# Kernel optimization log

Hardware: AMD Instinct MI355X
Metric: run time of the kernel (lower is better)

## Reference

```python
import jax, jax.numpy as jnp
import numpy as np

BS, EMB, RES = 256, 768, 14
N_MASKS, HID, OUT, N_PROJ = 16, 4096, 256, 4
BN_EPS = 1e-5


def setup_inputs() -> dict:
    key = jax.random.key(0)
    ks = jax.random.split(key, 8)
    x = jax.random.normal(ks[0], (BS, EMB, RES, RES), jnp.float32)
    # binary ROI masks over the 14x14 = 196 patch grid
    masks = (jax.random.uniform(ks[1], (BS, N_MASKS, RES * RES)) < 0.3).astype(jnp.float32)
    projection_idx = jax.random.randint(ks[2], (N_MASKS,), 0, N_PROJ, jnp.int32)
    mask_ids = jax.random.randint(ks[3], (BS, N_MASKS), 0, 100, jnp.int32)
    # stacked params for the N_PROJ MLP projectors
    W1 = jax.random.normal(ks[4], (N_PROJ, EMB, HID), jnp.float32) * 0.02
    b1 = jnp.zeros((N_PROJ, HID), jnp.float32)
    gamma = jnp.ones((N_PROJ, HID), jnp.float32)
    beta = jnp.zeros((N_PROJ, HID), jnp.float32)
    W2 = jax.random.normal(ks[5], (N_PROJ, HID, OUT), jnp.float32) * 0.02
    b2 = jnp.zeros((N_PROJ, OUT), jnp.float32)
    return {"x": x, "masks": masks, "projection_idx": projection_idx,
            "mask_ids": mask_ids, "W1": W1, "b1": b1, "gamma": gamma,
            "beta": beta, "W2": W2, "b2": b2}


def reference(x, masks, projection_idx, mask_ids, W1, b1, gamma, beta, W2, b2):
    bs, emb, hx, hy = x.shape
    # [bs, emb, hx, hy] -> [bs, hw, emb]
    emb_local = jnp.transpose(x, (0, 2, 3, 1)).reshape(bs, hx * hy, emb)
    # mask-normalized pooling:  pooled[b,n,:] = mean of embeddings inside mask n
    area = masks.sum(axis=-1, keepdims=True)
    smpl = masks / jnp.maximum(area, 1.0)
    pooled = smpl @ emb_local                       # [bs, n_masks, emb]
    # dense dispatch: run EVERY projector over all pooled tokens (as original)
    h = jnp.einsum('bne,peh->pbnh', pooled, W1) + b1[:, None, None, :]
    # BatchNorm1d in training mode over flattened (bs*n_masks) batch, per projector
    mu = h.mean(axis=(1, 2), keepdims=True)
    var = jnp.mean(jnp.square(h - mu), axis=(1, 2), keepdims=True)  # biased var
    h = (h - mu) * jax.lax.rsqrt(var + BN_EPS) * gamma[:, None, None, :] + beta[:, None, None, :]
    h = jax.nn.relu(h)
    o = jnp.einsum('pbnh,pho->pbno', h, W2) + b2[:, None, None, :]   # [P, bs, n, out]
    # keep only projector projection_idx[n] for mask-slot n (disjoint selection)
    n_proj = W1.shape[0]
    sel = (projection_idx[None, :] == jnp.arange(n_proj)[:, None]).astype(o.dtype)  # [P, n]
    xs = (o * sel[:, None, :, None]).sum(axis=0)     # [bs, n_masks, out]
    return (xs, mask_ids)
```

## Files before the change

### kernel.cpp

```cpp
#include <hip/hip_runtime.h>
#include <hip/hip_bf16.h>

#define BS 256
#define EMB 768
#define HW 196
#define NMASK 16
#define HID 4096
#define OUT 256
#define NPROJ 4
#define MROWS 4096

typedef __attribute__((ext_vector_type(8))) short bf16x8;
typedef __attribute__((ext_vector_type(4))) float f32x4;
typedef __attribute__((ext_vector_type(8))) unsigned short u16x8;

__device__ inline float bf2f(unsigned short u) {
    unsigned int x = ((unsigned int)u) << 16;
    return __builtin_bit_cast(float, x);
}
__device__ inline short f2bfs(float f) {
    return __builtin_bit_cast(short, __float2bfloat16(f));
}

#define GL16(gptr, lptr)                                                     \
    __builtin_amdgcn_global_load_lds(                                        \
        (const __attribute__((address_space(1))) void*)(gptr),               \
        (__attribute__((address_space(3))) void*)(lptr), 16, 0, 0)

__global__ __launch_bounds__(256) void fused_k1(
    const float* __restrict__ x, const float* __restrict__ masks,
    const float* __restrict__ W1, const float* __restrict__ W2,
    __hip_bfloat16* __restrict__ pooledG,
    __hip_bfloat16* __restrict__ W1T, __hip_bfloat16* __restrict__ W2T,
    float* __restrict__ mpB)
{
    __shared__ __align__(16) char smu[16704];
    const int bid = blockIdx.x, tid = threadIdx.x;

    if (bid < 1024) {
        short* afr = (short*)smu;
        float* inv = (float*)(smu + 14592);
        const int ec = bid & 3, b = bid >> 2;
        const float* mb = masks + (size_t)b * NMASK * HW;

        for (int s = tid; s < 7 * 64; s += 256) {
            int m = s & 15, kb = ((s >> 4) & 3) * 8 + (s >> 6) * 32;
            short v[8];
            #pragma unroll
            for (int j = 0; j < 8; ++j) {
                int kk = kb + j;
                v[j] = (kk < HW) ? f2bfs(mb[m * HW + kk]) : (short)0;
            }
            #pragma unroll
            for (int j = 0; j < 8; ++j) afr[s * 8 + j] = v[j];
        }
        if (tid >= 192) {
            int l = tid - 192, m = l >> 2, q = l & 3;
            float a = 0.f;
            for (int hw = q; hw < HW; hw += 4) a += mb[m * HW + hw];
            a += __shfl_xor(a, 1);
            a += __shfl_xor(a, 2);
            if (q == 0) inv[m] = 1.0f / fmaxf(a, 1.0f);
        }
        __syncthreads();

        const int lane = tid & 63, w = tid >> 6;
        const int lc = lane & 15, l4 = lane >> 4;
        const int ebase = ec * 192 + w * 48;
        const bf16x8* afv = (const bf16x8*)afr;
        f32x4 acc[3] = {};

        const float* xb0 = x + ((size_t)b * EMB + ebase + lc) * HW;

        for (int kc = 0; kc < 6; ++kc) {
            bf16x8 af = afv[kc * 64 + lane];
            float4 u[3][2];
            #pragma unroll
            for (int t = 0; t < 3; ++t) {
                const float* xr = xb0 + (size_t)(t * 16) * HW + kc * 32 + l4 * 8;
                u[t][0] = *(const float4*)(xr);
                u[t][1] = *(const float4*)(xr + 4);
            }
            #pragma unroll
            for (int t = 0; t < 3; ++t) {
                bf16x8 bf;
                bf[0] = f2bfs(u[t][0].x); bf[1] = f2bfs(u[t][0].y);
                bf[2] = f2bfs(u[t][0].z); bf[3] = f2bfs(u[t][0].w);
                bf[4] = f2bfs(u[t][1].x); bf[5] = f2bfs(u[t][1].y);
                bf[6] = f2bfs(u[t][1].z); bf[7] = f2bfs(u[t][1].w);
                acc[t] = __builtin_amdgcn_mfma_f32_16x16x32_bf16(af, bf, acc[t], 0, 0, 0);
            }
        }
        {
            bf16x8 af = afv[6 * 64 + lane];
            #pragma unroll
            for (int t = 0; t < 3; ++t) {
                bf16x8 bf = {};
                if (l4 == 0) {
                    float4 u0 = *(const float4*)(xb0 + (size_t)(t * 16) * HW + 192);
                    bf[0] = f2bfs(u0.x); bf[1] = f2bfs(u0.y);
                    bf[2] = f2bfs(u0.z); bf[3] = f2bfs(u0.w);
                }
                acc[t] = __builtin_amdgcn_mfma_f32_16x16x32_bf16(af, bf, acc[t], 0, 0, 0);
            }
        }

        #pragma unroll
        for (int t = 0; t < 3; ++t) {
            int e = ebase + t * 16 + lc;
            float msum = 0.f;
            #pragma unroll
            for (int j = 0; j < 4; ++j) {
                int m = l4 * 4 + j;
                float v = acc[t][j] * inv[m];
                msum += v;
                pooledG[((size_t)m * 256 + b) * EMB + e] = __float2bfloat16(v);
            }
            msum += __shfl_xor(msum, 16);
            msum += __shfl_xor(msum, 32);
            if (l4 == 0) mpB[(size_t)b * EMB + e] = msum;
        }
    } else {
        const float* src; __hip_bfloat16* dst; int R, C, xx, yy, z;
        if (bid < 4096) { int idx = bid - 1024; z = idx / 768; int r = idx % 768;
                          xx = r % 64; yy = r / 64; src = W1; dst = W1T; R = EMB; C = HID; }
        else            { int idx = bid - 4096; z = idx / 256; int r = idx % 256;
                          xx = r % 4;  yy = r / 4;  src = W2; dst = W2T; R = HID; C = OUT; }
        float (*tile)[65] = (float(*)[65])smu;
        const float* s = src + (size_t)z * R * C;
        __hip_bfloat16* d = dst + (size_t)z * R * C;
        const int c0 = xx * 64, r0 = yy * 64;
        for (int i = tid; i < 4096; i += 256) {
            int r = i >> 6, c = i & 63;
            tile[r][c] = s[(size_t)(r0 + r) * C + c0 + c];
        }
        __syncthreads();
        for (int i = tid; i < 4096; i += 256) {
            int c = i >> 6, r = i & 63;
            d[(size_t)(c0 + c) * R + r0 + r] = __float2bfloat16(tile[r][c]);
        }
    }
}

__global__ __launch_bounds__(256) void pgT_kernel(
    const __hip_bfloat16* __restrict__ src, __hip_bfloat16* __restrict__ dst)
{
    __shared__ __hip_bfloat16 tile[64][65];
    const int c0 = blockIdx.x * 64, r0 = blockIdx.y * 64, tid = threadIdx.x;
    for (int i = tid; i < 4096; i += 256) {
        int r = i >> 6, c = i & 63;
        tile[r][c] = src[(size_t)(r0 + r) * EMB + c0 + c];
    }
    __syncthreads();
    for (int i = tid; i < 4096; i += 256) {
        int c = i >> 6, r = i & 63;
        dst[(size_t)(c0 + c) * MROWS + r0 + r] = tile[r][c];
    }
}

__global__ __launch_bounds__(256) void cgemm(
    const __hip_bfloat16* __restrict__ PT, float* __restrict__ Cpart)
{
    __shared__ __align__(16) __hip_bfloat16 As[128 * 32];
    __shared__ __align__(16) __hip_bfloat16 Bs[128 * 32];
    const int tid = threadIdx.x, lane = tid & 63, wid = tid >> 6;
    const int n0 = blockIdx.x * 128, m0 = blockIdx.y * 128, kbase = blockIdx.z * 512;
    float* Cp = Cpart + (size_t)blockIdx.z * EMB * EMB;
    const int wr = wid >> 1, wc = wid & 1;
    const int l4 = lane >> 4, lc = lane & 15;

    f32x4 acc[4][4] = {};
    for (int k0 = kbase; k0 < kbase + 512; k0 += 32) {
        __syncthreads();
        #pragma unroll
        for (int r = 0; r < 2; ++r) {
            int t = r * 256 + tid;
            int row = t >> 2, ko = (t & 3) * 8;
            GL16(PT + (size_t)(m0 + row) * MROWS + k0 + ko, &As[(r * 256 + wid * 64) * 8]);
        }
        #pragma unroll
        for (int r = 0; r < 2; ++r) {
            int t = r * 256 + tid;
            int row = t >> 2, ko = (t & 3) * 8;
            GL16(PT + (size_t)(n0 + row) * MROWS + k0 + ko, &Bs[(r * 256 + wid * 64) * 8]);
        }
        __syncthreads();
        const bf16x8* Av = (const bf16x8*)As;
        const bf16x8* Bv = (const bf16x8*)Bs;
        bf16x8 a[4], b[4];
        #pragma unroll
        for (int m = 0; m < 4; ++m) a[m] = Av[(wr * 64 + m * 16 + lc) * 4 + l4];
        #pragma unroll
        for (int n = 0; n < 4; ++n) b[n] = Bv[(wc * 64 + n * 16 + lc) * 4 + l4];
        #pragma unroll
        for (int m = 0; m < 4; ++m)
            #pragma unroll
            for (int n = 0; n < 4; ++n)
                acc[m][n] = __builtin_amdgcn_mfma_f32_16x16x32_bf16(a[m], b[n], acc[m][n], 0, 0, 0);
    }
    #pragma unroll
    for (int m = 0; m < 4; ++m)
        #pragma unroll
        for (int n = 0; n < 4; ++n)
            #pragma unroll
            for (int j = 0; j < 4; ++j) {
                int row = m0 + wr * 64 + m * 16 + l4 * 4 + j;
                int col = n0 + wc * 64 + n * 16 + lc;
                Cp[(size_t)row * EMB + col] = acc[m][n][j];
            }
}

__global__ __launch_bounds__(256) void cvt_c(
    const float* __restrict__ Cpart, const float* __restrict__ mpB,
    __hip_bfloat16* __restrict__ Cbf, float* __restrict__ mp)
{
    const int bid = blockIdx.x, tid = threadIdx.x;
    if (bid < 576) {
        int i = (bid * 256 + tid) * 4;
        float sx = 0.f, sy = 0.f, sz = 0.f, sw = 0.f;
        #pragma unroll
        for (int kz = 0; kz < 8; ++kz) {
            float4 v = *(const float4*)(Cpart + (size_t)kz * EMB * EMB + i);
            sx += v.x; sy += v.y; sz += v.z; sw += v.w;
        }
        const float s = 1.0f / 4096.0f;
        Cbf[i + 0] = __float2bfloat16(sx * s);
        Cbf[i + 1] = __float2bfloat16(sy * s);
        Cbf[i + 2] = __float2bfloat16(sz * s);
        Cbf[i + 3] = __float2bfloat16(sw * s);
    } else {
        int e = (bid - 576) * 256 + tid;
        float s = 0.f;
        for (int b = 0; b < 256; ++b) s += mpB[(size_t)b * EMB + e];
        mp[e] = s * (1.0f / 4096.0f);
    }
}

__global__ __launch_bounds__(256) void ugemm(
    const __hip_bfloat16* __restrict__ W1T, const __hip_bfloat16* __restrict__ Cbf,
    const float* __restrict__ mp,
    float* __restrict__ Eh2p, float* __restrict__ Mup)
{
    __shared__ __align__(16) __hip_bfloat16 As[128 * 32];
    __shared__ __align__(16) __hip_bfloat16 Bs[128 * 32];
    const int tid = threadIdx.x, lane = tid & 63, wid = tid >> 6;
    const int n0 = blockIdx.x * 128, m0 = blockIdx.y * 128, p = blockIdx.z;
    const __hip_bfloat16* Ap = W1T + (size_t)p * HID * EMB;
    const int wr = wid >> 1, wc = wid & 1;
    const int l4 = lane >> 4, lc = lane & 15;

    f32x4 acc[4][4] = {};
    for (int k0 = 0; k0 < EMB; k0 += 32) {
        __syncthreads();
        #pragma unroll
        for (int r = 0; r < 2; ++r) {
            int t = r * 256 + tid;
            int row = t >> 2, ko = (t & 3) * 8;
            GL16(Ap + (size_t)(m0 + row) * EMB + k0 + ko, &As[(r * 256 + wid * 64) * 8]);
        }
        #pragma unroll
        for (int r = 0; r < 2; ++r) {
            int t = r * 256 + tid;
            int row = t >> 2, ko = (t & 3) * 8;
            GL16(Cbf + (size_t)(n0 + row) * EMB + k0 + ko, &Bs[(r * 256 + wid * 64) * 8]);
        }
        __syncthreads();
        const bf16x8* Av = (const bf16x8*)As;
        const bf16x8* Bv = (const bf16x8*)Bs;
        bf16x8 a[4], b[4];
        #pragma unroll
        for (int m = 0; m < 4; ++m) a[m] = Av[(wr * 64 + m * 16 + lc) * 4 + l4];
        #pragma unroll
        for (int n = 0; n < 4; ++n) b[n] = Bv[(wc * 64 + n * 16 + lc) * 4 + l4];
        #pragma unroll
        for (int m = 0; m < 4; ++m)
            #pragma unroll
            for (int n = 0; n < 4; ++n)
                acc[m][n] = __builtin_amdgcn_mfma_f32_16x16x32_bf16(a[m], b[n], acc[m][n], 0, 0, 0);
    }

    float mpv[4];
    #pragma unroll
    for (int n = 0; n < 4; ++n) mpv[n] = mp[n0 + wc * 64 + n * 16 + lc];
    #pragma unroll
    for (int m = 0; m < 4; ++m) {
        #pragma unroll
        for (int j = 0; j < 4; ++j) {
            int row = m0 + wr * 64 + m * 16 + l4 * 4 + j;
            const __hip_bfloat16* wrow = Ap + (size_t)row * EMB;
            float e2 = 0.f, mu = 0.f;
            #pragma unroll
            for (int n = 0; n < 4; ++n) {
                int col = n0 + wc * 64 + n * 16 + lc;
                float wv = bf2f(__builtin_bit_cast(unsigned short, wrow[col]));
                e2 += acc[m][n][j] * wv;
                mu += mpv[n] * wv;
            }
            e2 += __shfl_xor(e2, 1); e2 += __shfl_xor(e2, 2);
            e2 += __shfl_xor(e2, 4); e2 += __shfl_xor(e2, 8);
            mu += __shfl_xor(mu, 1); mu += __shfl_xor(mu, 2);
            mu += __shfl_xor(mu, 4); mu += __shfl_xor(mu, 8);
            if (lc == 0) {
                size_t idx = (((size_t)blockIdx.x * 2 + wc) * NPROJ + p) * HID + row;
                Eh2p[idx] = e2;
                Mup [idx] = mu;
            }
        }
    }
}

__global__ __launch_bounds__(512, 2) void gemm1_sel(
    const __hip_bfloat16* __restrict__ A, const __hip_bfloat16* __restrict__ W1T,
    const int* __restrict__ proj,
    const float* __restrict__ Eh2p, const float* __restrict__ Mup,
    const float* __restrict__ gamma, const float* __restrict__ beta,
    __hip_bfloat16* __restrict__ hrelu)
{
    __shared__ __align__(16) short LS[3 * 16384];
    __shared__ float sS[256], sT[256];
    const int tid = threadIdx.x, lane = tid & 63, w = tid >> 6;
    const int wr = w >> 2, wc = w & 3;
    const int lc = lane & 15, l4 = lane >> 4;
    const int n0 = blockIdx.x * 256, m0 = blockIdx.y * 256;
    const int p = proj[blockIdx.y];
    const __hip_bfloat16* Ag = A;
    const __hip_bfloat16* Bg = W1T + (size_t)p * HID * EMB;
    const bf16x8* LSv = (const bf16x8*)LS;

    if (tid < 256) {
        int col = n0 + tid;
        float e2 = 0.f, mu = 0.f;
        #pragma unroll
        for (int s = 0; s < 12; ++s) {
            e2 += Eh2p[((size_t)s * NPROJ + p) * HID + col];
            mu += Mup [((size_t)s * NPROJ + p) * HID + col];
        }
        float var = e2 - mu * mu;
        float is  = rsqrtf(fmaxf(var, 0.0f) + 1e-5f);
        float sc  = gamma[p * HID + col] * is;
        sS[tid] = sc;
        sT[tid] = beta[p * HID + col] - mu * sc;
    }

    auto STAGE = [&](int t) {
        const int sb = (t % 3) * 32768;
        #pragma unroll
        for (int ab = 0; ab < 2; ++ab) {
            const __hip_bfloat16* g = ab ? Bg : Ag;
            const int rbase = ab ? n0 : m0;
            #pragma unroll
            for (int i = 0; i < 2; ++i) {
                int c = (w * 2 + i) * 64 + lane;
                int row = c >> 2, ps = c & 3;
                int ls = ps ^ (row & 3);
                const __hip_bfloat16* src =
                    g + (size_t)(rbase + row) * EMB + t * 32 + ls * 8;
                GL16(src, (char*)LS + sb + ab * 16384 + (w * 2 + i) * 1024);
            }
        }
    };

    f32x4 acc[8][4] = {};

    STAGE(0);
    STAGE(1);
    asm volatile("s_waitcnt vmcnt(4)" ::: "memory");
    __builtin_amdgcn_s_barrier();

    for (int t = 0; t < 24; ++t) {
        if (t + 2 < 24) STAGE(t + 2);
        const int vb = (t % 3) * 2048;

        bf16x8 bfr[4];
        #pragma unroll
        for (int nf = 0; nf < 4; ++nf) {
            int rb = wc * 64 + nf * 16 + lc;
            bfr[nf] = LSv[vb + 1024 + rb * 4 + (l4 ^ (rb & 3))];
        }
        #pragma unroll
        for (int q = 0; q < 4; ++q) {
            bf16x8 afr[2];
            #pragma unroll
            for (int m2 = 0; m2 < 2; ++m2) {
                int ra = wr * 128 + (q * 2 + m2) * 16 + lc;
                afr[m2] = LSv[vb + ra * 4 + (l4 ^ (ra & 3))];
            }
            __builtin_amdgcn_s_setprio(1);
            #pragma unroll
            for (int m2 = 0; m2 < 2; ++m2)
                #pragma unroll
                for (int nf = 0; nf < 4; ++nf)
                    acc[q * 2 + m2][nf] = __builtin_amdgcn_mfma_f32_16x16x32_bf16(
                        afr[m2], bfr[nf], acc[q * 2 + m2][nf], 0, 0, 0);
            __builtin_amdgcn_s_setprio(0);
        }

        if (t + 2 < 24) {
            asm volatile("s_waitcnt vmcnt(4)" ::: "memory");
            __builtin_amdgcn_s_barrier();
        } else if (t + 2 == 24) {
            asm volatile("s_waitcnt vmcnt(0)" ::: "memory");
            __builtin_amdgcn_s_barrier();
        }
    }

    #pragma unroll
    for (int nf = 0; nf < 4; ++nf) {
        int cl = wc * 64 + nf * 16 + lc;
        int col = n0 + cl;
        float s = sS[cl];
        float tt = sT[cl];
        #pragma unroll
        for (int mf = 0; mf < 8; ++mf)
            #pragma unroll
            for (int j = 0; j < 4; ++j) {
                int row = m0 + wr * 128 + mf * 16 + l4 * 4 + j;
                float v = fmaxf(acc[mf][nf][j] * s + tt, 0.0f);
                hrelu[(size_t)row * HID + col] = __float2bfloat16(v);
            }
    }
}

__global__ __launch_bounds__(256) void gemm2(
    const __hip_bfloat16* __restrict__ Hn, const __hip_bfloat16* __restrict__ W2T,
    const int* __restrict__ proj, float* __restrict__ Opart)
{
    __shared__ __align__(16) __hip_bfloat16 As[128 * 32];
    __shared__ __align__(16) __hip_bfloat16 Bs[128 * 32];
    const int tid = threadIdx.x, lane = tid & 63, wid = tid >> 6;
    const int nmask = blockIdx.x;
    const int bc    = blockIdx.y;
    const int ct    = blockIdx.z >> 2, kz = blockIdx.z & 3;
    const int p = proj[nmask];
    const __hip_bfloat16* Ap = Hn + (size_t)(nmask * 256 + bc * 128) * HID;
    const __hip_bfloat16* Bp = W2T + ((size_t)p * OUT + ct * 128) * HID;
    float* Op = Opart + (size_t)kz * MROWS * OUT;
    const int wr = wid >> 1, wc = wid & 1;
    const int l4 = lane >> 4, lc = lane & 15;

    f32x4 acc[4][4] = {};
    for (int k0 = kz * 1024; k0 < kz * 1024 + 1024; k0 += 32) {
        __syncthreads();
        #pragma unroll
        for (int r = 0; r < 2; ++r) {
            int t = r * 256 + tid;
            int row = t >> 2, ko = (t & 3) * 8;
            GL16(Ap + (size_t)row * HID + k0 + ko, &As[(r * 256 + wid * 64) * 8]);
        }
        #pragma unroll
        for (int r = 0; r < 2; ++r) {
            int t = r * 256 + tid;
            int row = t >> 2, ko = (t & 3) * 8;
            GL16(Bp + (size_t)row * HID + k0 + ko, &Bs[(r * 256 + wid * 64) * 8]);
        }
        __syncthreads();
        const bf16x8* Av = (const bf16x8*)As;
        const bf16x8* Bv = (const bf16x8*)Bs;
        bf16x8 a[4], b[4];
        #pragma unroll
        for (int m = 0; m < 4; ++m) a[m] = Av[(wr * 64 + m * 16 + lc) * 4 + l4];
        #pragma unroll
        for (int n = 0; n < 4; ++n) b[n] = Bv[(wc * 64 + n * 16 + lc) * 4 + l4];
        #pragma unroll
        for (int m = 0; m < 4; ++m)
            #pragma unroll
            for (int n = 0; n < 4; ++n)
                acc[m][n] = __builtin_amdgcn_mfma_f32_16x16x32_bf16(a[m], b[n], acc[m][n], 0, 0, 0);
    }

    #pragma unroll
    for (int m = 0; m < 4; ++m)
        #pragma unroll
        for (int n = 0; n < 4; ++n)
            #pragma unroll
            for (int j = 0; j < 4; ++j) {
                int bb = bc * 128 + wr * 64 + m * 16 + l4 * 4 + j;
                int oc = ct * 128 + wc * 64 + n * 16 + lc;
                Op[((size_t)bb * NMASK + nmask) * OUT + oc] = acc[m][n][j];
            }
}

__global__ __launch_bounds__(256) void reduce_out(
    const float* __restrict__ Opart, const float* __restrict__ b2,
    const int* __restrict__ proj, const int* __restrict__ mids,
    float* __restrict__ out)
{
    int i = (blockIdx.x * 256 + threadIdx.x) * 4;
    float sx = 0.f, sy = 0.f, sz = 0.f, sw = 0.f;
    #pragma unroll
    for (int kz = 0; kz < 4; ++kz) {
        float4 v = *(const float4*)(Opart + (size_t)kz * MROWS * OUT + i);
        sx += v.x; sy += v.y; sz += v.z; sw += v.w;
    }
    int nm = (i >> 8) & 15;
    int p  = proj[nm];
    float4 bv = *(const float4*)(b2 + p * OUT + (i & 255));
    float4 r;
    r.x = sx + bv.x; r.y = sy + bv.y; r.z = sz + bv.z; r.w = sw + bv.w;
    *(float4*)(out + i) = r;
    if (blockIdx.x < 16) {
        int t = blockIdx.x * 256 + threadIdx.x;
        out[(size_t)MROWS * OUT + t] = (float)mids[t];
    }
}

extern "C" void kernel_launch(void* const* d_in, const int* in_sizes, int n_in,
                              void* d_out, int out_size, void* d_ws, size_t ws_size,
                              hipStream_t stream)
{
    const float* x     = (const float*)d_in[0];
    const float* masks = (const float*)d_in[1];
    const int*   proj  = (const int*)d_in[2];
    const int*   mids  = (const int*)d_in[3];
    const float* W1    = (const float*)d_in[4];
    const float* gamma = (const float*)d_in[6];
    const float* beta  = (const float*)d_in[7];
    const float* W2    = (const float*)d_in[8];
    const float* b2    = (const float*)d_in[9];
    float* out = (float*)d_out;

    char* ws = (char*)d_ws;
    __hip_bfloat16* pooledG = (__hip_bfloat16*)(ws);
    __hip_bfloat16* W1T     = (__hip_bfloat16*)(ws + 6291456);
    __hip_bfloat16* W2T     = (__hip_bfloat16*)(ws + 31457280);
    float*          mp      = (float*)(ws + 39845888);
    float*          Eh2p    = (float*)(ws + 39848960);
    float*          Mup     = (float*)(ws + 40635392);
    float*          mpB     = (float*)(ws + 41421824);
    char* R = ws + 42208256;
    __hip_bfloat16* pooledT = (__hip_bfloat16*)(R);
    float*          Cpart   = (float*)(R + 6291456);
    __hip_bfloat16* Cbf     = (__hip_bfloat16*)(R + 25165824);
    __hip_bfloat16* hrelu   = (__hip_bfloat16*)(R);
    float*          Opart   = (float*)(R + 33554432);

    fused_k1<<<5120, 256, 0, stream>>>(x, masks, W1, W2, pooledG, W1T, W2T, mpB);
    pgT_kernel<<<dim3(EMB / 64, MROWS / 64), 256, 0, stream>>>(pooledG, pooledT);
    cgemm<<<dim3(6, 6, 8), 256, 0, stream>>>(pooledT, Cpart);
    cvt_c<<<579, 256, 0, stream>>>(Cpart, mpB, Cbf, mp);
    ugemm<<<dim3(6, 32, 4), 256, 0, stream>>>(W1T, Cbf, mp, Eh2p, Mup);
    gemm1_sel<<<dim3(HID / 256, MROWS / 256), 512, 0, stream>>>(pooledG, W1T, proj, Eh2p, Mup, gamma, beta, hrelu);
    gemm2<<<dim3(NMASK, 2, 8), 256, 0, stream>>>(hrelu, W2T, proj, Opart);
    reduce_out<<<(MROWS * OUT) / 1024, 256, 0, stream>>>(Opart, b2, proj, mids, out);
}
```

Baseline: 213.6 us.

## Split pooling into LDS-staged kernel and merge weight/pooled transposes into prep

```diff
diff --git a/kernel.cpp b/kernel.cpp
--- a/kernel.cpp
+++ b/kernel.cpp
@@ -27,109 +27,122 @@
         (const __attribute__((address_space(1))) void*)(gptr),               \
         (__attribute__((address_space(3))) void*)(lptr), 16, 0, 0)
 
-__global__ __launch_bounds__(256) void fused_k1(
+__global__ __launch_bounds__(256) void pool2(
     const float* __restrict__ x, const float* __restrict__ masks,
+    __hip_bfloat16* __restrict__ pooledG, float* __restrict__ mpB)
+{
+    __shared__ __align__(16) float xs[192 * 196];
+    __shared__ __align__(16) short afr[7 * 64 * 8];
+    __shared__ float inv[NMASK];
+    const int ec = blockIdx.x & 3, b = blockIdx.x >> 2;
+    const int tid = threadIdx.x, lane = tid & 63, w = tid >> 6;
+    const float* mb = masks + (size_t)b * NMASK * HW;
+
+    {
+        const char* gsrc = (const char*)(x + ((size_t)b * EMB + ec * 192 + w * 48) * HW);
+        char* ldst = (char*)xs + w * 37632;
+        #pragma unroll
+        for (int i = 0; i < 36; ++i)
+            GL16(gsrc + (size_t)i * 1024 + (size_t)lane * 16, ldst + i * 1024);
+        if (lane < 48)
+            GL16(gsrc + (size_t)36 * 1024 + (size_t)lane * 16, ldst + 36 * 1024);
+    }
+
+    for (int s = tid; s < 7 * 64; s += 256) {
+        int m = s & 15, kb = ((s >> 4) & 3) * 8 + (s >> 6) * 32;
+        short v[8];
+        #pragma unroll
+        for (int j = 0; j < 8; ++j) {
+            int kk = kb + j;
+            v[j] = (kk < HW) ? f2bfs(mb[m * HW + kk]) : (short)0;
+        }
+        #pragma unroll
+        for (int j = 0; j < 8; ++j) afr[s * 8 + j] = v[j];
+    }
+    if (tid >= 192) {
+        int l = tid - 192, m = l >> 2, q = l & 3;
+        float a = 0.f;
+        for (int hw = q; hw < HW; hw += 4) a += mb[m * HW + hw];
+        a += __shfl_xor(a, 1);
+        a += __shfl_xor(a, 2);
+        if (q == 0) inv[m] = 1.0f / fmaxf(a, 1.0f);
+    }
+    __syncthreads();
+
+    const int lc = lane & 15, l4 = lane >> 4;
+    const int ebase = ec * 192 + w * 48;
+    const float* xw = xs + (size_t)(w * 48) * 196;
+    const bf16x8* afv = (const bf16x8*)afr;
+    f32x4 acc[3] = {};
+
+    for (int kc = 0; kc < 6; ++kc) {
+        bf16x8 af = afv[kc * 64 + lane];
+        float4 u[3][2];
+        #pragma unroll
+        for (int t = 0; t < 3; ++t) {
+            const float* xr = xw + (size_t)(t * 16 + lc) * 196 + kc * 32 + l4 * 8;
+            u[t][0] = *(const float4*)(xr);
+            u[t][1] = *(const float4*)(xr + 4);
+        }
+        #pragma unroll
+        for (int t = 0; t < 3; ++t) {
+            bf16x8 bf;
+            bf[0] = f2bfs(u[t][0].x); bf[1] = f2bfs(u[t][0].y);
+            bf[2] = f2bfs(u[t][0].z); bf[3] = f2bfs(u[t][0].w);
+            bf[4] = f2bfs(u[t][1].x); bf[5] = f2bfs(u[t][1].y);
+            bf[6] = f2bfs(u[t][1].z); bf[7] = f2bfs(u[t][1].w);
+            acc[t] = __builtin_amdgcn_mfma_f32_16x16x32_bf16(af, bf, acc[t], 0, 0, 0);
+        }
+    }
+    {
+        bf16x8 af = afv[6 * 64 + lane];
+        #pragma unroll
+        for (int t = 0; t < 3; ++t) {
+            bf16x8 bf = {};
+            if (l4 == 0) {
+                float4 u0 = *(const float4*)(xw + (size_t)(t * 16 + lc) * 196 + 192);
+                bf[0] = f2bfs(u0.x); bf[1] = f2bfs(u0.y);
+                bf[2] = f2bfs(u0.z); bf[3] = f2bfs(u0.w);
+            }
+            acc[t] = __builtin_amdgcn_mfma_f32_16x16x32_bf16(af, bf, acc[t], 0, 0, 0);
+        }
+    }
+
+    #pragma unroll
+    for (int t = 0; t < 3; ++t) {
+        int e = ebase + t * 16 + lc;
+        float msum = 0.f;
+        #pragma unroll
+        for (int j = 0; j < 4; ++j) {
+            int m = l4 * 4 + j;
+            float v = acc[t][j] * inv[m];
+            msum += v;
+            pooledG[((size_t)m * 256 + b) * EMB + e] = __float2bfloat16(v);
+        }
+        msum += __shfl_xor(msum, 16);
+        msum += __shfl_xor(msum, 32);
+        if (l4 == 0) mpB[(size_t)b * EMB + e] = msum;
+    }
+}
+
+__global__ __launch_bounds__(256) void prep(
     const float* __restrict__ W1, const float* __restrict__ W2,
-    __hip_bfloat16* __restrict__ pooledG,
+    const __hip_bfloat16* __restrict__ pg,
     __hip_bfloat16* __restrict__ W1T, __hip_bfloat16* __restrict__ W2T,
-    float* __restrict__ mpB)
-{
-    __shared__ __align__(16) char smu[16704];
+    __hip_bfloat16* __restrict__ pgT)
+{
+    __shared__ __align__(16) char sm[64 * 65 * 4];
     const int bid = blockIdx.x, tid = threadIdx.x;
-
-    if (bid < 1024) {
-        short* afr = (short*)smu;
-        float* inv = (float*)(smu + 14592);
-        const int ec = bid & 3, b = bid >> 2;
-        const float* mb = masks + (size_t)b * NMASK * HW;
-
-        for (int s = tid; s < 7 * 64; s += 256) {
-            int m = s & 15, kb = ((s >> 4) & 3) * 8 + (s >> 6) * 32;
-            short v[8];
-            #pragma unroll
-            for (int j = 0; j < 8; ++j) {
-                int kk = kb + j;
-                v[j] = (kk < HW) ? f2bfs(mb[m * HW + kk]) : (short)0;
-            }
-            #pragma unroll
-            for (int j = 0; j < 8; ++j) afr[s * 8 + j] = v[j];
-        }
-        if (tid >= 192) {
-            int l = tid - 192, m = l >> 2, q = l & 3;
-            float a = 0.f;
-            for (int hw = q; hw < HW; hw += 4) a += mb[m * HW + hw];
-            a += __shfl_xor(a, 1);
-            a += __shfl_xor(a, 2);
-            if (q == 0) inv[m] = 1.0f / fmaxf(a, 1.0f);
-        }
-        __syncthreads();
-
-        const int lane = tid & 63, w = tid >> 6;
-        const int lc = lane & 15, l4 = lane >> 4;
-        const int ebase = ec * 192 + w * 48;
-        const bf16x8* afv = (const bf16x8*)afr;
-        f32x4 acc[3] = {};
-
-        const float* xb0 = x + ((size_t)b * EMB + ebase + lc) * HW;
-
-        for (int kc = 0; kc < 6; ++kc) {
-            bf16x8 af = afv[kc * 64 + lane];
-            float4 u[3][2];
-            #pragma unroll
-            for (int t = 0; t < 3; ++t) {
-                const float* xr = xb0 + (size_t)(t * 16) * HW + kc * 32 + l4 * 8;
-                u[t][0] = *(const float4*)(xr);
-                u[t][1] = *(const float4*)(xr + 4);
-            }
-            #pragma unroll
-            for (int t = 0; t < 3; ++t) {
-                bf16x8 bf;
-                bf[0] = f2bfs(u[t][0].x); bf[1] = f2bfs(u[t][0].y);
-                bf[2] = f2bfs(u[t][0].z); bf[3] = f2bfs(u[t][0].w);
-                bf[4] = f2bfs(u[t][1].x); bf[5] = f2bfs(u[t][1].y);
-                bf[6] = f2bfs(u[t][1].z); bf[7] = f2bfs(u[t][1].w);
-                acc[t] = __builtin_amdgcn_mfma_f32_16x16x32_bf16(af, bf, acc[t], 0, 0, 0);
-            }
-        }
-        {
-            bf16x8 af = afv[6 * 64 + lane];
-            #pragma unroll
-            for (int t = 0; t < 3; ++t) {
-                bf16x8 bf = {};
-                if (l4 == 0) {
-                    float4 u0 = *(const float4*)(xb0 + (size_t)(t * 16) * HW + 192);
-                    bf[0] = f2bfs(u0.x); bf[1] = f2bfs(u0.y);
-                    bf[2] = f2bfs(u0.z); bf[3] = f2bfs(u0.w);
-                }
-                acc[t] = __builtin_amdgcn_mfma_f32_16x16x32_bf16(af, bf, acc[t], 0, 0, 0);
-            }
-        }
-
-        #pragma unroll
-        for (int t = 0; t < 3; ++t) {
-            int e = ebase + t * 16 + lc;
-            float msum = 0.f;
-            #pragma unroll
-            for (int j = 0; j < 4; ++j) {
-                int m = l4 * 4 + j;
-                float v = acc[t][j] * inv[m];
-                msum += v;
-                pooledG[((size_t)m * 256 + b) * EMB + e] = __float2bfloat16(v);
-            }
-            msum += __shfl_xor(msum, 16);
-            msum += __shfl_xor(msum, 32);
-            if (l4 == 0) mpB[(size_t)b * EMB + e] = msum;
-        }
-    } else {
-        const float* src; __hip_bfloat16* dst; int R, C, xx, yy, z;
-        if (bid < 4096) { int idx = bid - 1024; z = idx / 768; int r = idx % 768;
-                          xx = r % 64; yy = r / 64; src = W1; dst = W1T; R = EMB; C = HID; }
-        else            { int idx = bid - 4096; z = idx / 256; int r = idx % 256;
-                          xx = r % 4;  yy = r / 4;  src = W2; dst = W2T; R = HID; C = OUT; }
-        float (*tile)[65] = (float(*)[65])smu;
+    if (bid < 4096) {
+        const float* src; __hip_bfloat16* dst; int R, C, x, y, z;
+        if (bid < 3072) { z = bid / 768; int r = bid % 768; x = r % 64; y = r / 64;
+                          src = W1; dst = W1T; R = EMB; C = HID; }
+        else            { int b2 = bid - 3072; z = b2 / 256; int r = b2 % 256;
+                          x = r % 4; y = r / 4; src = W2; dst = W2T; R = HID; C = OUT; }
+        float (*tile)[65] = (float(*)[65])sm;
         const float* s = src + (size_t)z * R * C;
         __hip_bfloat16* d = dst + (size_t)z * R * C;
-        const int c0 = xx * 64, r0 = yy * 64;
+        const int c0 = x * 64, r0 = y * 64;
         for (int i = tid; i < 4096; i += 256) {
             int r = i >> 6, c = i & 63;
             tile[r][c] = s[(size_t)(r0 + r) * C + c0 + c];
@@ -139,22 +152,20 @@
             int c = i >> 6, r = i & 63;
             d[(size_t)(c0 + c) * R + r0 + r] = __float2bfloat16(tile[r][c]);
         }
-    }
-}
-
-__global__ __launch_bounds__(256) void pgT_kernel(
-    const __hip_bfloat16* __restrict__ src, __hip_bfloat16* __restrict__ dst)
-{
-    __shared__ __hip_bfloat16 tile[64][65];
-    const int c0 = blockIdx.x * 64, r0 = blockIdx.y * 64, tid = threadIdx.x;
-    for (int i = tid; i < 4096; i += 256) {
-        int r = i >> 6, c = i & 63;
-        tile[r][c] = src[(size_t)(r0 + r) * EMB + c0 + c];
-    }
-    __syncthreads();
-    for (int i = tid; i < 4096; i += 256) {
-        int c = i >> 6, r = i & 63;
-        dst[(size_t)(c0 + c) * MROWS + r0 + r] = tile[r][c];
+    } else {
+        const int b3 = bid - 4096;
+        const int x = b3 % 12, y = b3 / 12;
+        __hip_bfloat16 (*tile)[65] = (__hip_bfloat16(*)[65])sm;
+        const int c0 = x * 64, r0 = y * 64;
+        for (int i = tid; i < 4096; i += 256) {
+            int r = i >> 6, c = i & 63;
+            tile[r][c] = pg[(size_t)(r0 + r) * EMB + c0 + c];
+        }
+        __syncthreads();
+        for (int i = tid; i < 4096; i += 256) {
+            int c = i >> 6, r = i & 63;
+            pgT[(size_t)(c0 + c) * MROWS + r0 + r] = tile[r][c];
+        }
     }
 }
 
@@ -534,8 +545,8 @@
     __hip_bfloat16* hrelu   = (__hip_bfloat16*)(R);
     float*          Opart   = (float*)(R + 33554432);
 
-    fused_k1<<<5120, 256, 0, stream>>>(x, masks, W1, W2, pooledG, W1T, W2T, mpB);
-    pgT_kernel<<<dim3(EMB / 64, MROWS / 64), 256, 0, stream>>>(pooledG, pooledT);
+    pool2<<<1024, 256, 0, stream>>>(x, masks, pooledG, mpB);
+    prep<<<4864, 256, 0, stream>>>(W1, W2, pooledG, W1T, W2T, pooledT);
     cgemm<<<dim3(6, 6, 8), 256, 0, stream>>>(pooledT, Cpart);
     cvt_c<<<579, 256, 0, stream>>>(Cpart, mpB, Cbf, mp);
     ugemm<<<dim3(6, 32, 4), 256, 0, stream>>>(W1T, Cbf, mp, Eh2p, Mup);
```

Result: slower. 221.1 us (+3.5%).
